# Performance work log

Measured on AMD Instinct MI355X. Metric: run time of the kernel, lower is better.

Reference implementation:

```python
import jax, jax.numpy as jnp
import numpy as np

CONTACT_THRESH = 0.01
COLLISION_THRESH = 0.005
WEIGHT_PEN = 100.0
WEIGHT_MISS = 10.0
# MANO fingertip + palm contact-zone vertex indices (hardcoded in module)
CONTACT_IDX = np.array([745, 317, 444, 556, 673, 95, 182, 234, 279, 320])

SCALE = 0.1  # place points in a 0.1 m cube so mm-scale thresholds are meaningful


def setup_inputs() -> dict:
    key = jax.random.key(0)
    k1, k2, k3, k4 = jax.random.split(key, 4)
    B, NH, V = 8, 778, 40000
    hand_verts = jax.random.uniform(k1, (B, NH, 3), dtype=jnp.float32) * SCALE
    obj_verts = jax.random.uniform(k2, (B, V, 3), dtype=jnp.float32) * SCALE
    hand_faces = jax.random.randint(k3, (1538, 3), 0, NH, dtype=jnp.int64 if jax.config.read('jax_enable_x64') else jnp.int32)
    obj_faces = jax.random.randint(k4, (79996, 3), 0, V, dtype=jnp.int64 if jax.config.read('jax_enable_x64') else jnp.int32)
    return {"hand_verts": hand_verts, "obj_verts": obj_verts,
            "hand_faces": hand_faces, "obj_faces": obj_faces}


def _min_dists(a, b):
    """Brute-force 1-NN: min Euclidean distance from each point in a [B,N,3] to b [B,M,3] -> [B,N]."""
    a_sq = jnp.sum(a * a, axis=-1, keepdims=True)          # [B,N,1]
    b_sq = jnp.sum(b * b, axis=-1)                          # [B,M]
    ab = jnp.einsum('bnd,bmd->bnm', a, b)                   # [B,N,M]
    d2 = jnp.maximum(a_sq + b_sq[:, None, :] - 2.0 * ab, 0.0)
    return jnp.sqrt(jnp.min(d2, axis=2))                    # [B,N]


def _masked_mean(vals, mask):
    cnt = jnp.sum(mask)
    s = jnp.sum(jnp.where(mask, vals, 0.0))
    return jnp.where(cnt > 0, s / jnp.maximum(cnt, 1).astype(vals.dtype), jnp.zeros((), vals.dtype))


def reference(hand_verts, obj_verts, hand_faces, obj_faces):
    # faces are unused by the loss (as in the torch module)
    idx = jnp.asarray(CONTACT_IDX)
    # distances are computed under no_grad / detached in the original
    dists = jax.lax.stop_gradient(_min_dists(hand_verts, obj_verts))              # [B,778]
    contact_dists = jax.lax.stop_gradient(_min_dists(hand_verts[:, idx, :], obj_verts))  # [B,10]

    pen_mask = dists < COLLISION_THRESH
    pen_loss = _masked_mean((COLLISION_THRESH - dists) ** 2, pen_mask)

    att_mask = (contact_dists > COLLISION_THRESH) & (contact_dists < CONTACT_THRESH)
    att_loss = _masked_mean(contact_dists ** 2, att_mask)

    contact_loss = WEIGHT_PEN * pen_loss + WEIGHT_MISS * att_loss
    dist_mean = jnp.mean(dists)
    num_contacts = jnp.sum(att_mask).astype(jnp.int32)
    num_penetrations = jnp.sum(pen_mask).astype(jnp.int32)
    return (contact_loss, pen_loss, att_loss, dist_mean, num_contacts, num_penetrations)
```

## Files before the change

kernel.cpp:

```cpp
#include <hip/hip_runtime.h>
#include <math.h>

constexpr int NH    = 778;
constexpr int GRIDC = 16;
constexpr int NCELL = GRIDC * GRIDC * GRIDC;
constexpr int CAP   = 40;
constexpr float CELL     = 0.1f / GRIDC;
constexpr float INV_CELL = GRIDC / 0.1f;
constexpr int NXCD = 8;
constexpr int NSH  = 64;


struct alignas(64) Shard {
    double sd, sp, sa;
    int cp, ca;
    int pad[3];
};

__device__ __forceinline__ int clampc(int v) {
    return min(GRIDC - 1, max(0, v));
}

__global__ __launch_bounds__(256) void bin_kernel(
    const float* __restrict__ obj,
    int* __restrict__ cnt,
    int* __restrict__ ocnt,
    float4* __restrict__ buckets,
    float4* __restrict__ ovf,
    int B, int V, int bpb)
{
    const int w = (blockIdx.x % NXCD) * (gridDim.x / NXCD) + blockIdx.x / NXCD;
    const int b = w / bpb;
    if (b >= B) return;
    const int p0 = ((w % bpb) * 256 + (int)threadIdx.x) * 4;
    if (p0 >= V) return;

    float px[4], py[4], pz[4];
    int np;
    const size_t fbase = ((size_t)b * V + p0) * 3;
    if (p0 + 4 <= V && (fbase & 3) == 0) {
        const float4* src = (const float4*)(obj + fbase);
        const float4 A = src[0], Bv = src[1], C = src[2];
        px[0]=A.x;  py[0]=A.y;  pz[0]=A.z;
        px[1]=A.w;  py[1]=Bv.x; pz[1]=Bv.y;
        px[2]=Bv.z; py[2]=Bv.w; pz[2]=C.x;
        px[3]=C.y;  py[3]=C.z;  pz[3]=C.w;
        np = 4;
    } else {
        np = min(4, V - p0);
        for (int q = 0; q < np; ++q) {
            px[q] = obj[fbase + 3 * q + 0];
            py[q] = obj[fbase + 3 * q + 1];
            pz[q] = obj[fbase + 3 * q + 2];
        }
    }

    const int cb = b * NCELL;
#pragma unroll
    for (int q = 0; q < 4; ++q) {
        if (q >= np) break;
        const int cx = clampc((int)(px[q] * INV_CELL));
        const int cy = clampc((int)(py[q] * INV_CELL));
        const int cz = clampc((int)(pz[q] * INV_CELL));
        const int cell = cb + (cz * GRIDC + cy) * GRIDC + cx;
        const int idx = atomicAdd(&cnt[cell], 1);
        if (idx < CAP) {
            buckets[(size_t)cell * CAP + idx] = make_float4(px[q], py[q], pz[q], 0.f);
        } else {
            const int oi = atomicAdd(ocnt, 1);
            ovf[oi] = make_float4(px[q], py[q], pz[q], __int_as_float(b));
        }
    }
}

__global__ __launch_bounds__(256) void query_kernel(
    const float* __restrict__ hand,
    const int* __restrict__ cnt,
    const float4* __restrict__ buckets,
    const float4* __restrict__ ovf,
    const int* __restrict__ ocnt,
    Shard* __restrict__ shards,
    int B, int bpq)
{
    constexpr float COLL = 0.005f;
    constexpr float CONT = 0.01f;
    const int tid  = threadIdx.x;
    const int wave = tid >> 6;
    const int lane = tid & 63;
    const int w  = (blockIdx.x % NXCD) * (gridDim.x / NXCD) + blockIdx.x / NXCD;
    const int b  = w / bpq;
    const int ql = (w % bpq) * 4 + wave;
    const bool valid = (b < B) && (ql < NH);

    float best = 3.4e38f;

    if (valid) {
        const int i = b * NH + ql;
        const float hx = hand[3 * i + 0];
        const float hy = hand[3 * i + 1];
        const float hz = hand[3 * i + 2];
        const int hcx = clampc((int)(hx * INV_CELL));
        const int hcy = clampc((int)(hy * INV_CELL));
        const int hcz = clampc((int)(hz * INV_CELL));
        const int cbase = b * NCELL;

        if (lane < 54) {
            const int cl  = lane >> 1;
            const int sub = lane & 1;
            const int cx = hcx + (cl % 3) - 1;
            const int cy = hcy + ((cl / 3) % 3) - 1;
            const int cz = hcz + (cl / 9) - 1;
            if (cx >= 0 && cx < GRIDC && cy >= 0 && cy < GRIDC &&
                cz >= 0 && cz < GRIDC) {
                const int cell = cbase + (cz * GRIDC + cy) * GRIDC + cx;
                const int n = min(cnt[cell], CAP);
                const float4* bp = buckets + (size_t)cell * CAP;
                for (int k = sub; k < n; k += 2) {
                    const float4 p = bp[k];
                    const float dx = p.x - hx, dy = p.y - hy, dz = p.z - hz;
                    best = fminf(best, fmaf(dx, dx, fmaf(dy, dy, dz * dz)));
                }
            }
        }

        const int on = *ocnt;
        for (int k = lane; k < on; k += 64) {
            const float4 p = ovf[k];
            if (__float_as_int(p.w) == b) {
                const float dx = p.x - hx, dy = p.y - hy, dz = p.z - hz;
                best = fminf(best, fmaf(dx, dx, fmaf(dy, dy, dz * dz)));
            }
        }

#pragma unroll
        for (int d = 1; d < 64; d <<= 1) best = fminf(best, __shfl_xor(best, d));

        for (int r = 2; r < GRIDC; ++r) {
            const float bnd = (float)(r - 1) * CELL;
            if (best <= bnd * bnd) break;
            const int side = 2 * r + 1;
            const int ncells = side * side * side;
            for (int ci = lane; ci < ncells; ci += 64) {
                const int dx = ci % side - r;
                const int dy = (ci / side) % side - r;
                const int dz = ci / (side * side) - r;
                if (max(max(abs(dx), abs(dy)), abs(dz)) != r) continue;
                const int cx = hcx + dx, cy = hcy + dy, cz = hcz + dz;
                if (cx < 0 || cx >= GRIDC || cy < 0 || cy >= GRIDC ||
                    cz < 0 || cz >= GRIDC) continue;
                const int cell = cbase + (cz * GRIDC + cy) * GRIDC + cx;
                const int n = min(cnt[cell], CAP);
                const float4* bp = buckets + (size_t)cell * CAP;
                for (int k = 0; k < n; ++k) {
                    const float4 p = bp[k];
                    const float ddx = p.x - hx, ddy = p.y - hy, ddz = p.z - hz;
                    best = fminf(best, fmaf(ddx, ddx, fmaf(ddy, ddy, ddz * ddz)));
                }
            }
#pragma unroll
            for (int d = 1; d < 64; d <<= 1) best = fminf(best, __shfl_xor(best, d));
        }
    }

    __shared__ double ssd[4], ssp[4], ssa[4];
    __shared__ int scp[4], sca[4];
    if (lane == 0) {
        double sd = 0.0, sp = 0.0, sa = 0.0;
        int cp = 0, ca = 0;
        if (valid) {
            const float d = sqrtf(fmaxf(best, 0.f));
            sd = (double)d;
            if (d < COLL) { const float t = COLL - d; sp = (double)(t * t); cp = 1; }
            const bool isc = (ql == 745) | (ql == 317) | (ql == 444) | (ql == 556) |
                             (ql == 673) | (ql == 95)  | (ql == 182) | (ql == 234) |
                             (ql == 279) | (ql == 320);
            if (isc & (d > COLL) & (d < CONT)) { sa = (double)(d * d); ca = 1; }
        }
        ssd[wave] = sd; ssp[wave] = sp; ssa[wave] = sa;
        scp[wave] = cp; sca[wave] = ca;
    }
    __syncthreads();
    if (tid == 0) {
        const double sd = ssd[0] + ssd[1] + ssd[2] + ssd[3];
        const double sp = ssp[0] + ssp[1] + ssp[2] + ssp[3];
        const double sa = ssa[0] + ssa[1] + ssa[2] + ssa[3];
        const int cp = scp[0] + scp[1] + scp[2] + scp[3];
        const int ca = sca[0] + sca[1] + sca[2] + sca[3];
        Shard* s = &shards[blockIdx.x & (NSH - 1)];
        atomicAdd(&s->sd, sd);
        atomicAdd(&s->sp, sp);
        atomicAdd(&s->sa, sa);
        atomicAdd(&s->cp, cp);
        atomicAdd(&s->ca, ca);
    }
}

__global__ __launch_bounds__(64) void finalize_tiny(
    const Shard* __restrict__ shards, float* __restrict__ out, int nq)
{
    const int l = threadIdx.x;
    double sd = shards[l].sd, sp = shards[l].sp, sa = shards[l].sa;
    int cp = shards[l].cp, ca = shards[l].ca;
#pragma unroll
    for (int d = 1; d < 64; d <<= 1) {
        sd += __shfl_xor(sd, d);
        sp += __shfl_xor(sp, d);
        sa += __shfl_xor(sa, d);
        cp += __shfl_xor(cp, d);
        ca += __shfl_xor(ca, d);
    }
    if (l == 0) {
        const double pen_loss = cp > 0 ? sp / (double)cp : 0.0;
        const double att_loss = ca > 0 ? sa / (double)ca : 0.0;
        out[0] = (float)(100.0 * pen_loss + 10.0 * att_loss);
        out[1] = (float)pen_loss;
        out[2] = (float)att_loss;
        out[3] = (float)(sd / (double)nq);
        out[4] = (float)ca;
        out[5] = (float)cp;
    }
}

typedef float v2f __attribute__((ext_vector_type(2)));
constexpr int FT = 16, FG = 4, FBLK = 256, FCHUNK = 2560;
constexpr int FNBX = (NH + FG * FT - 1) / (FG * FT);
constexpr int FLPP = FCHUNK / FBLK, FPP = FLPP / 2;

__global__ __launch_bounds__(FBLK, 2) void nn_brute_kernel(
    const float* __restrict__ hand, const float* __restrict__ obj,
    unsigned int* __restrict__ minb, int V)
{
    __shared__ float s_red[4][16 * 65];
    const int bx = blockIdx.x, c = blockIdx.y, b = blockIdx.z;
    const int tid = threadIdx.x, wave = tid >> 6, lane = tid & 63;
    const int r = lane & 15, seg = lane >> 4;
    const float* ob = obj + (size_t)b * V * 3;
    const int base = c * FCHUNK + tid;
    v2f ox2[FPP], oy2[FPP], oz2[FPP], oq2[FPP];
#pragma unroll
    for (int p = 0; p < FPP; ++p) {
        const int ja = min(base + (2 * p + 0) * FBLK, V - 1);
        const int jb = min(base + (2 * p + 1) * FBLK, V - 1);
        const float xa = ob[3 * ja], ya = ob[3 * ja + 1], za = ob[3 * ja + 2];
        const float xb = ob[3 * jb], yb = ob[3 * jb + 1], zb = ob[3 * jb + 2];
        ox2[p] = (v2f){-2.f * xa, -2.f * xb};
        oy2[p] = (v2f){-2.f * ya, -2.f * yb};
        oz2[p] = (v2f){-2.f * za, -2.f * zb};
        oq2[p] = (v2f){fmaf(xa, xa, fmaf(ya, ya, za * za)),
                       fmaf(xb, xb, fmaf(yb, yb, zb * zb))};
    }
    const float* hb = hand + (size_t)b * NH * 3;
    float* sw = &s_red[wave][0];
#pragma unroll 1
    for (int g = 0; g < FG; ++g) {
        float hx[FT], hy[FT], hz[FT], m[FT];
#pragma unroll
        for (int t = 0; t < FT; ++t) {
            const int h = min((bx * FG + g) * FT + t, NH - 1);
            hx[t] = hb[3 * h]; hy[t] = hb[3 * h + 1]; hz[t] = hb[3 * h + 2];
            m[t] = 3.4e38f;
        }
#pragma unroll
        for (int p = 0; p < FPP; ++p) {
#pragma unroll
            for (int t = 0; t < FT; ++t) {
                v2f a = __builtin_elementwise_fma(ox2[p], (v2f){hx[t], hx[t]}, oq2[p]);
                a = __builtin_elementwise_fma(oy2[p], (v2f){hy[t], hy[t]}, a);
                a = __builtin_elementwise_fma(oz2[p], (v2f){hz[t], hz[t]}, a);
                m[t] = fminf(fminf(a.x, a.y), m[t]);
            }
        }
#pragma unroll
        for (int t = 0; t < FT; ++t) {
            const float hq = fmaf(hx[t], hx[t], fmaf(hy[t], hy[t], hz[t] * hz[t]));
            sw[t * 65 + lane] = m[t] + hq;
        }
        __builtin_amdgcn_wave_barrier();
        float v = 3.4e38f;
        const int rb = r * 65 + seg * 16;
#pragma unroll
        for (int j = 0; j < 16; ++j) v = fminf(v, sw[rb + j]);
        __builtin_amdgcn_wave_barrier();
        v = fminf(v, __shfl_xor(v, 16));
        v = fminf(v, __shfl_xor(v, 32));
        if (seg == 0) {
            const int hidx = (bx * FG + g) * FT + r;
            if (hidx < NH) {
                const unsigned bits = __float_as_uint(fmaxf(v, 0.f));
                unsigned int* p = &minb[b * NH + hidx];
                if (bits < *((volatile unsigned int*)p)) atomicMin(p, bits);
            }
        }
    }
}

__global__ __launch_bounds__(256) void finalize_kernel(
    const float* __restrict__ dist, float* __restrict__ out, int B)
{
    constexpr float COLL = 0.005f;
    constexpr float CONT = 0.01f;
    const int total = B * NH;
    const int tid = threadIdx.x;

    double sum_d = 0.0, pen_sum = 0.0, att_sum = 0.0;
    int pen_cnt = 0, att_cnt = 0;
    for (int i = tid; i < total; i += 256) {
        const float d = sqrtf(fmaxf(dist[i], 0.f));
        sum_d += (double)d;
        if (d < COLL) { const float t = COLL - d; pen_sum += (double)(t * t); pen_cnt++; }
        const int n = i % NH;
        const bool isc = (n == 745) | (n == 317) | (n == 444) | (n == 556) |
                         (n == 673) | (n == 95)  | (n == 182) | (n == 234) |
                         (n == 279) | (n == 320);
        if (isc & (d > COLL) & (d < CONT)) { att_sum += (double)(d * d); att_cnt++; }
    }

    __shared__ double sd[256], sp[256], sa[256];
    __shared__ int    cp[256], ca[256];
    sd[tid] = sum_d; sp[tid] = pen_sum; sa[tid] = att_sum;
    cp[tid] = pen_cnt; ca[tid] = att_cnt;
    __syncthreads();
    for (int off = 128; off > 0; off >>= 1) {
        if (tid < off) {
            sd[tid] += sd[tid + off]; sp[tid] += sp[tid + off];
            sa[tid] += sa[tid + off];
            cp[tid] += cp[tid + off]; ca[tid] += ca[tid + off];
        }
        __syncthreads();
    }
    if (tid == 0) {
        const double pen_loss = cp[0] > 0 ? sp[0] / (double)cp[0] : 0.0;
        const double att_loss = ca[0] > 0 ? sa[0] / (double)ca[0] : 0.0;
        out[0] = (float)(100.0 * pen_loss + 10.0 * att_loss);
        out[1] = (float)pen_loss;
        out[2] = (float)att_loss;
        out[3] = (float)(sd[0] / (double)total);
        out[4] = (float)ca[0];
        out[5] = (float)cp[0];
    }
}

extern "C" void kernel_launch(void* const* d_in, const int* in_sizes, int n_in,
                              void* d_out, int out_size, void* d_ws, size_t ws_size,
                              hipStream_t stream) {
    const float* hand = (const float*)d_in[0];
    const float* obj  = (const float*)d_in[1];

    const int B = in_sizes[0] / (NH * 3);
    const int V = in_sizes[1] / (B * 3);
    const int total = B * V;
    const int nq = B * NH;

    char* base = (char*)d_ws;
    size_t off = 65536;
    Shard* shards = (Shard*)(base + off);
    int*   ocnt   = (int*)(base + off + 4096);
    int*   cnt    = (int*)(base + off + 8192);
    const size_t cnt_bytes = (size_t)B * NCELL * sizeof(int);
    const size_t boff = (off + 8192 + cnt_bytes + 255) & ~(size_t)255;
    float4* buckets = (float4*)(base + boff);
    const size_t bkt_bytes = (size_t)B * NCELL * CAP * sizeof(float4);
    float4* ovf = (float4*)(base + boff + bkt_bytes);
    const size_t need = boff + bkt_bytes + (size_t)total * sizeof(float4);

    if (ws_size >= need) {
        hipMemsetAsync(base + off, 0, 8192 + cnt_bytes, stream);

        const int bpb = (V + 1023) / 1024;
        int gbin = B * bpb; gbin = (gbin + NXCD - 1) & ~(NXCD - 1);
        bin_kernel<<<gbin, 256, 0, stream>>>(obj, cnt, ocnt, buckets, ovf,
                                             B, V, bpb);

        const int bpq = (NH + 3) / 4;
        int gq = B * bpq; gq = (gq + NXCD - 1) & ~(NXCD - 1);
        query_kernel<<<gq, 256, 0, stream>>>(hand, cnt, buckets, ovf, ocnt,
                                             shards, B, bpq);

        finalize_tiny<<<1, 64, 0, stream>>>(shards, (float*)d_out, nq);
    } else {
        hipMemsetAsync(d_ws, 0x7F, (size_t)nq * sizeof(unsigned int), stream);
        dim3 grid(FNBX, (V + FCHUNK - 1) / FCHUNK, B);
        nn_brute_kernel<<<grid, FBLK, 0, stream>>>(hand, obj,
                                                   (unsigned int*)d_ws, V);
        finalize_kernel<<<1, 256, 0, stream>>>((const float*)d_ws, (float*)d_out, B);
    }
}
```

Measured before the change: 88.43 us.

## Fuse memset, binning, query and finalize into one cooperative persistent kernel

Replaces the memset plus three kernel launches with a single cooperative-launch kernel that zeroes the counters, bins object points, runs the nearest-neighbour queries and does the final reduction, separated by grid-wide syncs. Each block is tied to one batch and loops over points and hand vertices persistently. The first-ring cell loads are also issued speculatively, a fixed number per lane, so the fetches overlap. This is meant to remove launch gaps and the memset, in exchange for grid.sync overhead and less parallelism in the query phase.

Result: slower. 317.7 us (+259.3%).

```diff
diff --git a/kernel.cpp b/kernel.cpp
--- a/kernel.cpp
+++ b/kernel.cpp
@@ -1,5 +1,8 @@
 #include <hip/hip_runtime.h>
+#include <hip/hip_cooperative_groups.h>
 #include <math.h>
+
+namespace cg = cooperative_groups;
 
 constexpr int NH    = 778;
 constexpr int GRIDC = 16;
@@ -9,6 +12,7 @@
 constexpr float INV_CELL = GRIDC / 0.1f;
 constexpr int NXCD = 8;
 constexpr int NSH  = 64;
+constexpr int SPEC = 8;
 
 
 struct alignas(64) Shard {
@@ -21,20 +25,11 @@
     return min(GRIDC - 1, max(0, v));
 }
 
-__global__ __launch_bounds__(256) void bin_kernel(
-    const float* __restrict__ obj,
-    int* __restrict__ cnt,
-    int* __restrict__ ocnt,
-    float4* __restrict__ buckets,
-    float4* __restrict__ ovf,
-    int B, int V, int bpb)
-{
-    const int w = (blockIdx.x % NXCD) * (gridDim.x / NXCD) + blockIdx.x / NXCD;
-    const int b = w / bpb;
-    if (b >= B) return;
-    const int p0 = ((w % bpb) * 256 + (int)threadIdx.x) * 4;
-    if (p0 >= V) return;
-
+__device__ __forceinline__ void bin4(
+    const float* __restrict__ obj, int* __restrict__ cnt, int* __restrict__ ocnt,
+    float4* __restrict__ buckets, float4* __restrict__ ovf,
+    int b, int V, int p0)
+{
     float px[4], py[4], pz[4];
     int np;
     const size_t fbase = ((size_t)b * V + p0) * 3;
@@ -54,7 +49,6 @@
             pz[q] = obj[fbase + 3 * q + 2];
         }
     }
-
     const int cb = b * NCELL;
 #pragma unroll
     for (int q = 0; q < 4; ++q) {
@@ -73,17 +67,203 @@
     }
 }
 
-__global__ __launch_bounds__(256) void query_kernel(
-    const float* __restrict__ hand,
-    const int* __restrict__ cnt,
-    const float4* __restrict__ buckets,
-    const float4* __restrict__ ovf,
-    const int* __restrict__ ocnt,
-    Shard* __restrict__ shards,
-    int B, int bpq)
+__device__ float query_one(
+    const float* __restrict__ hand, const int* __restrict__ cnt,
+    const float4* __restrict__ buckets, const float4* __restrict__ ovf,
+    int on, int b, int i, int lane)
+{
+    const float hx = hand[3 * i + 0];
+    const float hy = hand[3 * i + 1];
+    const float hz = hand[3 * i + 2];
+    const int hcx = clampc((int)(hx * INV_CELL));
+    const int hcy = clampc((int)(hy * INV_CELL));
+    const int hcz = clampc((int)(hz * INV_CELL));
+    const int cbase = b * NCELL;
+
+    float best = 3.4e38f;
+
+    if (lane < 54) {
+        const int cl  = lane >> 1;
+        const int sub = lane & 1;
+        const int cx = hcx + (cl % 3) - 1;
+        const int cy = hcy + ((cl / 3) % 3) - 1;
+        const int cz = hcz + (cl / 9) - 1;
+        if (cx >= 0 && cx < GRIDC && cy >= 0 && cy < GRIDC &&
+            cz >= 0 && cz < GRIDC) {
+            const int cell = cbase + (cz * GRIDC + cy) * GRIDC + cx;
+            const float4* bp = buckets + (size_t)cell * CAP;
+            const int n = min(cnt[cell], CAP);
+            float4 e[SPEC];
+#pragma unroll
+            for (int j = 0; j < SPEC; ++j) e[j] = bp[sub + 2 * j];
+#pragma unroll
+            for (int j = 0; j < SPEC; ++j) {
+                if (sub + 2 * j < n) {
+                    const float dx = e[j].x - hx, dy = e[j].y - hy, dz = e[j].z - hz;
+                    best = fminf(best, fmaf(dx, dx, fmaf(dy, dy, dz * dz)));
+                }
+            }
+            for (int k = sub + 2 * SPEC; k < n; k += 2) {
+                const float4 p = bp[k];
+                const float dx = p.x - hx, dy = p.y - hy, dz = p.z - hz;
+                best = fminf(best, fmaf(dx, dx, fmaf(dy, dy, dz * dz)));
+            }
+        }
+    }
+
+    for (int k = lane; k < on; k += 64) {
+        const float4 p = ovf[k];
+        if (__float_as_int(p.w) == b) {
+            const float dx = p.x - hx, dy = p.y - hy, dz = p.z - hz;
+            best = fminf(best, fmaf(dx, dx, fmaf(dy, dy, dz * dz)));
+        }
+    }
+
+#pragma unroll
+    for (int d = 1; d < 64; d <<= 1) best = fminf(best, __shfl_xor(best, d));
+
+    for (int r = 2; r < GRIDC; ++r) {
+        const float bnd = (float)(r - 1) * CELL;
+        if (best <= bnd * bnd) break;
+        const int side = 2 * r + 1;
+        const int ncells = side * side * side;
+        for (int ci = lane; ci < ncells; ci += 64) {
+            const int dx = ci % side - r;
+            const int dy = (ci / side) % side - r;
+            const int dz = ci / (side * side) - r;
+            if (max(max(abs(dx), abs(dy)), abs(dz)) != r) continue;
+            const int cx = hcx + dx, cy = hcy + dy, cz = hcz + dz;
+            if (cx < 0 || cx >= GRIDC || cy < 0 || cy >= GRIDC ||
+                cz < 0 || cz >= GRIDC) continue;
+            const int cell = cbase + (cz * GRIDC + cy) * GRIDC + cx;
+            const int n = min(cnt[cell], CAP);
+            const float4* bp = buckets + (size_t)cell * CAP;
+            for (int k = 0; k < n; ++k) {
+                const float4 p = bp[k];
+                const float ddx = p.x - hx, ddy = p.y - hy, ddz = p.z - hz;
+                best = fminf(best, fmaf(ddx, ddx, fmaf(ddy, ddy, ddz * ddz)));
+            }
+        }
+#pragma unroll
+        for (int d = 1; d < 64; d <<= 1) best = fminf(best, __shfl_xor(best, d));
+    }
+    return best;
+}
+
+__device__ __forceinline__ void accum_stats(
+    float best, int ql, double& sd, double& sp, double& sa, int& cp, int& ca)
 {
     constexpr float COLL = 0.005f;
     constexpr float CONT = 0.01f;
+    const float d = sqrtf(fmaxf(best, 0.f));
+    sd += (double)d;
+    if (d < COLL) { const float t = COLL - d; sp += (double)(t * t); cp++; }
+    const bool isc = (ql == 745) | (ql == 317) | (ql == 444) | (ql == 556) |
+                     (ql == 673) | (ql == 95)  | (ql == 182) | (ql == 234) |
+                     (ql == 279) | (ql == 320);
+    if (isc & (d > COLL) & (d < CONT)) { sa += (double)(d * d); ca++; }
+}
+
+__global__ __launch_bounds__(256, 4) void mega_kernel(
+    const float* __restrict__ hand, const float* __restrict__ obj,
+    int* __restrict__ cnt, int* __restrict__ ocnt,
+    float4* __restrict__ buckets, float4* __restrict__ ovf,
+    Shard* __restrict__ shards, float* __restrict__ out,
+    int B, int V)
+{
+    cg::grid_group grid = cg::this_grid();
+    const int tid  = threadIdx.x;
+    const int wave = tid >> 6;
+    const int lane = tid & 63;
+    const int nblk = (int)gridDim.x;
+    const int gtid = (int)blockIdx.x * 256 + tid;
+    const int gthreads = nblk * 256;
+
+    const int ztot = B * NCELL;
+    for (int i = gtid; i < ztot; i += gthreads) cnt[i] = 0;
+    if (gtid < NSH) {
+        shards[gtid].sd = 0.0; shards[gtid].sp = 0.0; shards[gtid].sa = 0.0;
+        shards[gtid].cp = 0;   shards[gtid].ca = 0;
+    }
+    if (gtid == 0) *ocnt = 0;
+    grid.sync();
+
+    const int b    = (int)blockIdx.x % B;
+    const int rank = (int)blockIdx.x / B;
+    const int bpg  = nblk / B;
+    const int bt   = rank * 256 + tid;
+    const int bthreads = bpg * 256;
+    for (int p0 = bt * 4; p0 < V; p0 += bthreads * 4)
+        bin4(obj, cnt, ocnt, buckets, ovf, b, V, p0);
+    grid.sync();
+
+    const int on = *ocnt;
+    const int bwid = rank * 4 + wave;
+    const int bwaves = bpg * 4;
+    double asd = 0.0, asp = 0.0, asa = 0.0;
+    int acp = 0, aca = 0;
+    for (int ql = bwid; ql < NH; ql += bwaves) {
+        const float best = query_one(hand, cnt, buckets, ovf, on,
+                                     b, b * NH + ql, lane);
+        if (lane == 0) accum_stats(best, ql, asd, asp, asa, acp, aca);
+    }
+    __shared__ double ssd[4], ssp[4], ssa[4];
+    __shared__ int scp[4], sca[4];
+    if (lane == 0) { ssd[wave]=asd; ssp[wave]=asp; ssa[wave]=asa;
+                     scp[wave]=acp; sca[wave]=aca; }
+    __syncthreads();
+    if (tid == 0) {
+        Shard* s = &shards[blockIdx.x & (NSH - 1)];
+        atomicAdd(&s->sd, ssd[0]+ssd[1]+ssd[2]+ssd[3]);
+        atomicAdd(&s->sp, ssp[0]+ssp[1]+ssp[2]+ssp[3]);
+        atomicAdd(&s->sa, ssa[0]+ssa[1]+ssa[2]+ssa[3]);
+        atomicAdd(&s->cp, scp[0]+scp[1]+scp[2]+scp[3]);
+        atomicAdd(&s->ca, sca[0]+sca[1]+sca[2]+sca[3]);
+    }
+    grid.sync();
+
+    if (blockIdx.x == 0 && tid < 64) {
+        const int l = tid;
+        double sd = shards[l].sd, sp = shards[l].sp, sa = shards[l].sa;
+        int cp = shards[l].cp, ca = shards[l].ca;
+#pragma unroll
+        for (int d = 1; d < 64; d <<= 1) {
+            sd += __shfl_xor(sd, d); sp += __shfl_xor(sp, d);
+            sa += __shfl_xor(sa, d);
+            cp += __shfl_xor(cp, d); ca += __shfl_xor(ca, d);
+        }
+        if (l == 0) {
+            const double pen_loss = cp > 0 ? sp / (double)cp : 0.0;
+            const double att_loss = ca > 0 ? sa / (double)ca : 0.0;
+            out[0] = (float)(100.0 * pen_loss + 10.0 * att_loss);
+            out[1] = (float)pen_loss;
+            out[2] = (float)att_loss;
+            out[3] = (float)(sd / (double)(B * NH));
+            out[4] = (float)ca;
+            out[5] = (float)cp;
+        }
+    }
+}
+
+__global__ __launch_bounds__(256) void bin_kernel(
+    const float* __restrict__ obj, int* __restrict__ cnt, int* __restrict__ ocnt,
+    float4* __restrict__ buckets, float4* __restrict__ ovf,
+    int B, int V, int bpb)
+{
+    const int w = (blockIdx.x % NXCD) * (gridDim.x / NXCD) + blockIdx.x / NXCD;
+    const int b = w / bpb;
+    if (b >= B) return;
+    const int p0 = ((w % bpb) * 256 + (int)threadIdx.x) * 4;
+    if (p0 >= V) return;
+    bin4(obj, cnt, ocnt, buckets, ovf, b, V, p0);
+}
+
+__global__ __launch_bounds__(256) void query_kernel(
+    const float* __restrict__ hand, const int* __restrict__ cnt,
+    const float4* __restrict__ buckets, const float4* __restrict__ ovf,
+    const int* __restrict__ ocnt, Shard* __restrict__ shards,
+    int B, int bpq)
+{
     const int tid  = threadIdx.x;
     const int wave = tid >> 6;
     const int lane = tid & 63;
@@ -92,106 +272,25 @@
     const int ql = (w % bpq) * 4 + wave;
     const bool valid = (b < B) && (ql < NH);
 
-    float best = 3.4e38f;
-
+    double sd = 0.0, sp = 0.0, sa = 0.0;
+    int cp = 0, ca = 0;
     if (valid) {
-        const int i = b * NH + ql;
-        const float hx = hand[3 * i + 0];
-        const float hy = hand[3 * i + 1];
-        const float hz = hand[3 * i + 2];
-        const int hcx = clampc((int)(hx * INV_CELL));
-        const int hcy = clampc((int)(hy * INV_CELL));
-        const int hcz = clampc((int)(hz * INV_CELL));
-        const int cbase = b * NCELL;
-
-        if (lane < 54) {
-            const int cl  = lane >> 1;
-            const int sub = lane & 1;
-            const int cx = hcx + (cl % 3) - 1;
-            const int cy = hcy + ((cl / 3) % 3) - 1;
-            const int cz = hcz + (cl / 9) - 1;
-            if (cx >= 0 && cx < GRIDC && cy >= 0 && cy < GRIDC &&
-                cz >= 0 && cz < GRIDC) {
-                const int cell = cbase + (cz * GRIDC + cy) * GRIDC + cx;
-                const int n = min(cnt[cell], CAP);
-                const float4* bp = buckets + (size_t)cell * CAP;
-                for (int k = sub; k < n; k += 2) {
-                    const float4 p = bp[k];
-                    const float dx = p.x - hx, dy = p.y - hy, dz = p.z - hz;
-                    best = fminf(best, fmaf(dx, dx, fmaf(dy, dy, dz * dz)));
-                }
-            }
-        }
-
-        const int on = *ocnt;
-        for (int k = lane; k < on; k += 64) {
-            const float4 p = ovf[k];
-            if (__float_as_int(p.w) == b) {
-                const float dx = p.x - hx, dy = p.y - hy, dz = p.z - hz;
-                best = fminf(best, fmaf(dx, dx, fmaf(dy, dy, dz * dz)));
-            }
-        }
-
-#pragma unroll
-        for (int d = 1; d < 64; d <<= 1) best = fminf(best, __shfl_xor(best, d));
-
-        for (int r = 2; r < GRIDC; ++r) {
-            const float bnd = (float)(r - 1) * CELL;
-            if (best <= bnd * bnd) break;
-            const int side = 2 * r + 1;
-            const int ncells = side * side * side;
-            for (int ci = lane; ci < ncells; ci += 64) {
-                const int dx = ci % side - r;
-                const int dy = (ci / side) % side - r;
-                const int dz = ci / (side * side) - r;
-                if (max(max(abs(dx), abs(dy)), abs(dz)) != r) continue;
-                const int cx = hcx + dx, cy = hcy + dy, cz = hcz + dz;
-                if (cx < 0 || cx >= GRIDC || cy < 0 || cy >= GRIDC ||
-                    cz < 0 || cz >= GRIDC) continue;
-                const int cell = cbase + (cz * GRIDC + cy) * GRIDC + cx;
-                const int n = min(cnt[cell], CAP);
-                const float4* bp = buckets + (size_t)cell * CAP;
-                for (int k = 0; k < n; ++k) {
-                    const float4 p = bp[k];
-                    const float ddx = p.x - hx, ddy = p.y - hy, ddz = p.z - hz;
-                    best = fminf(best, fmaf(ddx, ddx, fmaf(ddy, ddy, ddz * ddz)));
-                }
-            }
-#pragma unroll
-            for (int d = 1; d < 64; d <<= 1) best = fminf(best, __shfl_xor(best, d));
-        }
-    }
-
+        const float best = query_one(hand, cnt, buckets, ovf, *ocnt,
+                                     b, b * NH + ql, lane);
+        if (lane == 0) accum_stats(best, ql, sd, sp, sa, cp, ca);
+    }
     __shared__ double ssd[4], ssp[4], ssa[4];
     __shared__ int scp[4], sca[4];
-    if (lane == 0) {
-        double sd = 0.0, sp = 0.0, sa = 0.0;
-        int cp = 0, ca = 0;
-        if (valid) {
-            const float d = sqrtf(fmaxf(best, 0.f));
-            sd = (double)d;
-            if (d < COLL) { const float t = COLL - d; sp = (double)(t * t); cp = 1; }
-            const bool isc = (ql == 745) | (ql == 317) | (ql == 444) | (ql == 556) |
-                             (ql == 673) | (ql == 95)  | (ql == 182) | (ql == 234) |
-                             (ql == 279) | (ql == 320);
-            if (isc & (d > COLL) & (d < CONT)) { sa = (double)(d * d); ca = 1; }
-        }
-        ssd[wave] = sd; ssp[wave] = sp; ssa[wave] = sa;
-        scp[wave] = cp; sca[wave] = ca;
-    }
+    if (lane == 0) { ssd[wave]=sd; ssp[wave]=sp; ssa[wave]=sa;
+                     scp[wave]=cp; sca[wave]=ca; }
     __syncthreads();
     if (tid == 0) {
-        const double sd = ssd[0] + ssd[1] + ssd[2] + ssd[3];
-        const double sp = ssp[0] + ssp[1] + ssp[2] + ssp[3];
-        const double sa = ssa[0] + ssa[1] + ssa[2] + ssa[3];
-        const int cp = scp[0] + scp[1] + scp[2] + scp[3];
-        const int ca = sca[0] + sca[1] + sca[2] + sca[3];
         Shard* s = &shards[blockIdx.x & (NSH - 1)];
-        atomicAdd(&s->sd, sd);
-        atomicAdd(&s->sp, sp);
-        atomicAdd(&s->sa, sa);
-        atomicAdd(&s->cp, cp);
-        atomicAdd(&s->ca, ca);
+        atomicAdd(&s->sd, ssd[0]+ssd[1]+ssd[2]+ssd[3]);
+        atomicAdd(&s->sp, ssp[0]+ssp[1]+ssp[2]+ssp[3]);
+        atomicAdd(&s->sa, ssa[0]+ssa[1]+ssa[2]+ssa[3]);
+        atomicAdd(&s->cp, scp[0]+scp[1]+scp[2]+scp[3]);
+        atomicAdd(&s->ca, sca[0]+sca[1]+sca[2]+sca[3]);
     }
 }
 
@@ -203,11 +302,9 @@
     int cp = shards[l].cp, ca = shards[l].ca;
 #pragma unroll
     for (int d = 1; d < 64; d <<= 1) {
-        sd += __shfl_xor(sd, d);
-        sp += __shfl_xor(sp, d);
+        sd += __shfl_xor(sd, d); sp += __shfl_xor(sp, d);
         sa += __shfl_xor(sa, d);
-        cp += __shfl_xor(cp, d);
-        ca += __shfl_xor(ca, d);
+        cp += __shfl_xor(cp, d); ca += __shfl_xor(ca, d);
     }
     if (l == 0) {
         const double pen_loss = cp > 0 ? sp / (double)cp : 0.0;
@@ -301,7 +398,6 @@
     constexpr float CONT = 0.01f;
     const int total = B * NH;
     const int tid = threadIdx.x;
-
     double sum_d = 0.0, pen_sum = 0.0, att_sum = 0.0;
     int pen_cnt = 0, att_cnt = 0;
     for (int i = tid; i < total; i += 256) {
@@ -314,7 +410,6 @@
                          (n == 279) | (n == 320);
         if (isc & (d > COLL) & (d < CONT)) { att_sum += (double)(d * d); att_cnt++; }
     }
-
     __shared__ double sd[256], sp[256], sa[256];
     __shared__ int    cp[256], ca[256];
     sd[tid] = sum_d; sp[tid] = pen_sum; sa[tid] = att_sum;
@@ -364,21 +459,51 @@
     const size_t need = boff + bkt_bytes + (size_t)total * sizeof(float4);
 
     if (ws_size >= need) {
-        hipMemsetAsync(base + off, 0, 8192 + cnt_bytes, stream);
-
-        const int bpb = (V + 1023) / 1024;
-        int gbin = B * bpb; gbin = (gbin + NXCD - 1) & ~(NXCD - 1);
-        bin_kernel<<<gbin, 256, 0, stream>>>(obj, cnt, ocnt, buckets, ovf,
-                                             B, V, bpb);
-
-        const int bpq = (NH + 3) / 4;
-        int gq = B * bpq; gq = (gq + NXCD - 1) & ~(NXCD - 1);
-        query_kernel<<<gq, 256, 0, stream>>>(hand, cnt, buckets, ovf, ocnt,
-                                             shards, B, bpq);
-
-        finalize_tiny<<<1, 64, 0, stream>>>(shards, (float*)d_out, nq);
+        static int s_nblk = 0;
+        if (s_nblk == 0) {
+            int dev = 0;
+            (void)hipGetDevice(&dev);
+            int coop = 0;
+            (void)hipDeviceGetAttribute(&coop, hipDeviceAttributeCooperativeLaunch, dev);
+            int perCU = 0;
+            if (hipOccupancyMaxActiveBlocksPerMultiprocessor(
+                    &perCU, mega_kernel, 256, 0) != hipSuccess || perCU <= 0)
+                perCU = 2;
+            int ncu = 0;
+            if (hipDeviceGetAttribute(&ncu, hipDeviceAttributeMultiprocessorCount,
+                                      dev) != hipSuccess || ncu <= 0)
+                ncu = 256;
+            s_nblk = coop ? perCU * ncu : -1;
+        }
+
+        int nblk = (s_nblk > 0) ? (s_nblk / B) * B : 0;
+        bool launched = false;
+        if (nblk >= B) {
+            float* outp = (float*)d_out;
+            int Bv = B, Vv = V;
+            void* kargs[] = {(void*)&hand, (void*)&obj, (void*)&cnt, (void*)&ocnt,
+                             (void*)&buckets, (void*)&ovf, (void*)&shards,
+                             (void*)&outp, (void*)&Bv, (void*)&Vv};
+            hipError_t ce = hipLaunchCooperativeKernel(
+                (const void*)mega_kernel, dim3(nblk), dim3(256), kargs, 0, stream);
+            if (ce == hipSuccess) launched = true;
+            else (void)hipGetLastError();
+        }
+
+        if (!launched) {
+            (void)hipMemsetAsync(base + off, 0, 8192 + cnt_bytes, stream);
+            const int bpb = (V + 1023) / 1024;
+            int gbin = B * bpb; gbin = (gbin + NXCD - 1) & ~(NXCD - 1);
+            bin_kernel<<<gbin, 256, 0, stream>>>(obj, cnt, ocnt, buckets, ovf,
+                                                 B, V, bpb);
+            const int bpq = (NH + 3) / 4;
+            int gq = B * bpq; gq = (gq + NXCD - 1) & ~(NXCD - 1);
+            query_kernel<<<gq, 256, 0, stream>>>(hand, cnt, buckets, ovf, ocnt,
+                                                 shards, B, bpq);
+            finalize_tiny<<<1, 64, 0, stream>>>(shards, (float*)d_out, nq);
+        }
     } else {
-        hipMemsetAsync(d_ws, 0x7F, (size_t)nq * sizeof(unsigned int), stream);
+        (void)hipMemsetAsync(d_ws, 0x7F, (size_t)nq * sizeof(unsigned int), stream);
         dim3 grid(FNBX, (V + FCHUNK - 1) / FCHUNK, B);
         nn_brute_kernel<<<grid, FBLK, 0, stream>>>(hand, obj,
                                                    (unsigned int*)d_ws, V);
```
